# Optimization experiments

Hardware: AMD Instinct MI355X
Metric: run time of the kernel (lower is better)

The kernel has to match this reference:

```python
import jax, jax.numpy as jnp
import numpy as np

B, NZ, L = 8, 16, 512
E, DM, NH, HD = 256, 512, 16, 32
FF, NL, E1D, PDIM, PMAX = 1024, 8, 32, 64, 24
EPS_LN = 1e-5
EPS_D = 1e-12


def _ln(x, g, b):
    m = jnp.mean(x, axis=-1, keepdims=True)
    v = jnp.mean((x - m) ** 2, axis=-1, keepdims=True)
    return (x - m) / jnp.sqrt(v + EPS_LN) * g + b


def setup_inputs() -> dict:
    key = jax.random.key(0)
    ks = iter(jax.random.split(key, 32))
    rn = lambda shape, fan: jax.random.normal(next(ks), shape, jnp.float32) / np.float32(np.sqrt(fan))
    inp = {
        "z": jax.random.normal(next(ks), (B, NZ, L), jnp.float32),
        "x": jax.random.uniform(next(ks), (B, 20, L), jnp.float32),
        # embeddings
        "pos_table": rn((2 * PMAX + 1, PDIM), 1.0),
        "aa_table": rn((20, E1D), 1.0),
        # embed_x: Linear(nz,E), relu, Linear(E,E)
        "ex_w1": rn((NZ, E), NZ), "ex_b1": jnp.zeros((E,), jnp.float32),
        "ex_w2": rn((E, E), E), "ex_b2": jnp.zeros((E,), jnp.float32),
        # per-layer stacked params
        "Wq": rn((NL, E, DM), E), "Wk": rn((NL, E, DM), E), "Wv": rn((NL, E, DM), E),
        "Wo": rn((NL, DM, E), DM), "bo": jnp.zeros((NL, E), jnp.float32),
        "W2d": rn((NL, PDIM, NH), PDIM), "b2d": jnp.zeros((NL, NH), jnp.float32),
        "W1": rn((NL, E + E1D, FF), E + E1D), "b1": jnp.zeros((NL, FF), jnp.float32),
        "W2": rn((NL, FF, E), FF), "b2": jnp.zeros((NL, E), jnp.float32),
        "g1": jnp.ones((NL, E), jnp.float32), "be1": jnp.zeros((NL, E), jnp.float32),
        "g2": jnp.ones((NL, E), jnp.float32), "be2": jnp.zeros((NL, E), jnp.float32),
        # mlp_3d: Linear(E,E), relu, Linear(E,3)
        "m3_w1": rn((E, E), E), "m3_b1": jnp.zeros((E,), jnp.float32),
        "m3_w2": rn((E, 3), E), "m3_b2": jnp.zeros((3,), jnp.float32),
    }
    return inp


def reference(z, x, pos_table, aa_table, ex_w1, ex_b1, ex_w2, ex_b2,
              Wq, Wk, Wv, Wo, bo, W2d, b2d, W1, b1, W2, b2,
              g1, be1, g2, be2, m3_w1, m3_b1, m3_w2, m3_b2):
    Bn, _, Ln = z.shape
    h = jnp.transpose(z, (0, 2, 1))  # (B, L, nz)
    # relative-position bins: argmin over integer bins == clip to [-PMAX, PMAX]
    rel = jnp.arange(Ln)[None, :] - jnp.arange(Ln)[:, None]
    bins = jnp.clip(rel, -PMAX, PMAX) + PMAX
    pe = pos_table[bins]  # (L, L, PDIM), batch-replicated
    e_aa = aa_table[jnp.argmax(x, axis=1)]  # (B, L, E1D)
    # embed_x MLP
    h = jax.nn.relu(h @ ex_w1 + ex_b1) @ ex_w2 + ex_b2  # (B, L, E)
    scale = np.float32(1.0 / np.sqrt(DM))  # dp_attn_norm='d_model'
    for i in range(NL):
        q = (h @ Wq[i]).reshape(Bn, Ln, NH, HD) * scale
        k = (h @ Wk[i]).reshape(Bn, Ln, NH, HD)
        v = (h @ Wv[i]).reshape(Bn, Ln, NH, HD)
        # learned pairwise bias: mlp_2d then transpose(1,3).transpose(2,3) -> bias[h,i,j] = out[i,j,h]
        bias = jnp.einsum('lmp,ph->hlm', pe, W2d[i]) + b2d[i][:, None, None]
        scores = jnp.einsum('blhd,bmhd->bhlm', q, k) + bias[None]
        attn = jax.nn.softmax(scores, axis=-1)
        o = jnp.einsum('bhlm,bmhd->blhd', attn, v).reshape(Bn, Ln, DM)
        h = _ln(h + (o @ Wo[i] + bo[i]), g1[i], be1[i])
        um = jnp.concatenate([h, e_aa], axis=-1)  # (B, L, E+E1D)
        s2 = jax.nn.relu(um @ W1[i] + b1[i]) @ W2[i] + b2[i]
        h = _ln(h + s2, g2[i], be2[i])
    r = jax.nn.relu(h @ m3_w1 + m3_b1) @ m3_w2 + m3_b2  # (B, L, 3)
    # distance map (get_coords=False path)
    d = jnp.sqrt(jnp.sum((r[:, None, :, :] - r[:, :, None, :]) ** 2, axis=-1) + EPS_D)
    return d  # (B, L, L)
```

## Files before the change

### kernel.cpp

```cpp
#include <hip/hip_runtime.h>
#include <math.h>

constexpr int Bn = 8, NZ = 16, Ln = 512;
constexpr int E = 256, DM = 512, NH = 16, HD = 32;
constexpr int FF = 1024, NL = 8, E1D = 32, PDIM = 64, PMAX = 24;
constexpr int ROWS = Bn * Ln;
constexpr float QSCALE = 0.04419417382415922f;

typedef __attribute__((ext_vector_type(8))) short bf16x8;
typedef __attribute__((ext_vector_type(4))) float floatx4;

__device__ inline unsigned short f2b(float f) {
  union { float f; unsigned u; } v; v.f = f;
  unsigned r = (v.u + 0x7FFF + ((v.u >> 16) & 1)) >> 16;
  return (unsigned short)r;
}
__device__ inline float b2f(unsigned short u) {
  union { unsigned u; float f; } v; v.u = ((unsigned)u) << 16; return v.f;
}

__global__ __launch_bounds__(256) void transpose_qkv(
    const float* __restrict__ Wq, const float* __restrict__ Wk,
    const float* __restrict__ Wv, unsigned short* __restrict__ qkvT)
{
  __shared__ float t[32][33];
  int zb = blockIdx.z;
  int which = zb / NL, l = zb % NL;
  const float* s = (which == 0 ? Wq : which == 1 ? Wk : Wv) + (size_t)l * E * DM;
  unsigned short* d = qkvT + (size_t)l * 3 * DM * E + (size_t)which * DM * E;
  int c0 = blockIdx.x * 32, r0 = blockIdx.y * 32;
  int tx = threadIdx.x & 31, ty = threadIdx.x >> 5;
  #pragma unroll
  for (int i = 0; i < 4; ++i)
    t[ty + i * 8][tx] = s[(size_t)(r0 + ty + i * 8) * DM + c0 + tx];
  __syncthreads();
  #pragma unroll
  for (int i = 0; i < 4; ++i)
    d[(size_t)(c0 + ty + i * 8) * E + r0 + tx] = f2b(t[tx][ty + i * 8]);
}

__global__ __launch_bounds__(256) void transpose_bf16(
    const float* __restrict__ src, unsigned short* __restrict__ dst,
    int R, int C, size_t sls, size_t dls)
{
  __shared__ float t[32][33];
  int l = blockIdx.z;
  int c0 = blockIdx.x * 32, r0 = blockIdx.y * 32;
  int tx = threadIdx.x & 31, ty = threadIdx.x >> 5;
  const float* s = src + (size_t)l * sls;
  unsigned short* d = dst + (size_t)l * dls;
  #pragma unroll
  for (int i = 0; i < 4; ++i)
    t[ty + i * 8][tx] = s[(size_t)(r0 + ty + i * 8) * C + c0 + tx];
  __syncthreads();
  #pragma unroll
  for (int i = 0; i < 4; ++i)
    d[(size_t)(c0 + ty + i * 8) * R + r0 + tx] = f2b(t[tx][ty + i * 8]);
}

__global__ __launch_bounds__(256) void embed1_kernel(
    const float* __restrict__ z, const float* __restrict__ x,
    const float* __restrict__ aa,
    const float* __restrict__ w1, const float* __restrict__ b1,
    float* __restrict__ t0, unsigned short* __restrict__ umb)
{
  int row = blockIdx.x;
  int b = row >> 9, l = row & (Ln - 1);
  int t = threadIdx.x;
  __shared__ float zs[NZ];
  __shared__ int am_s;
  if (t < NZ) zs[t] = z[((size_t)b * NZ + t) * Ln + l];
  if (t == 0) {
    const float* xp = x + (size_t)b * 20 * Ln + l;
    int am = 0; float bv = xp[0];
    for (int c = 1; c < 20; ++c) { float vv = xp[(size_t)c * Ln]; if (vv > bv) { bv = vv; am = c; } }
    am_s = am;
  }
  __syncthreads();
  float a1 = b1[t];
  #pragma unroll
  for (int nz = 0; nz < NZ; ++nz) a1 += zs[nz] * w1[nz * E + t];
  t0[(size_t)row * E + t] = fmaxf(a1, 0.f);
  if (t < E1D) umb[(size_t)row * (E + E1D) + E + t] = f2b(aa[am_s * E1D + t]);
}

__global__ __launch_bounds__(256) void bias_kernel(
    const float* __restrict__ pos, const float* __restrict__ W2d,
    const float* __restrict__ b2d, float* __restrict__ bias49)
{
  int layer = blockIdx.x;
  for (int idx = threadIdx.x; idx < NH * 49; idx += 256) {
    int hh = idx / 49, bin = idx % 49;
    float acc = b2d[layer * NH + hh];
    for (int p = 0; p < PDIM; ++p)
      acc += pos[bin * PDIM + p] * W2d[((size_t)layer * PDIM + p) * NH + hh];
    bias49[(size_t)layer * NH * 49 + hh * 49 + bin] = acc;
  }
}

template<int BM, int BN, bool BIAS, bool RELU, bool OUTBF16, bool QKV>
__global__ __launch_bounds__(256) void gemm_mfma(
    const unsigned short* __restrict__ A, const unsigned short* __restrict__ Bt,
    const float* __restrict__ bias,
    float* __restrict__ Cf, unsigned short* __restrict__ Cb, int N, int K)
{
  constexpr int MT = BM / 32, NT = BN / 32;
  __shared__ __align__(16) unsigned short As[BM][40];
  __shared__ __align__(16) unsigned short Bs[BN][40];
  const int tid = threadIdx.x;
  const int wave = tid >> 6, ln = tid & 63;
  const int quad = ln >> 4, l16 = ln & 15;
  const int wm = wave >> 1, wn = wave & 1;
  const int m0 = blockIdx.y * BM, n0 = blockIdx.x * BN;

  floatx4 acc[MT][NT] = {};

  for (int kb = 0; kb < K; kb += 32) {
    __syncthreads();
    #pragma unroll
    for (int it = 0; it < BM / 64; ++it) {
      int c = tid + it * 256;
      int row = c >> 2, cc = (c & 3) * 8;
      *(float4*)&As[row][cc] = *(const float4*)(A + (size_t)(m0 + row) * K + kb + cc);
    }
    #pragma unroll
    for (int it = 0; it < BN / 64; ++it) {
      int c = tid + it * 256;
      int row = c >> 2, cc = (c & 3) * 8;
      *(float4*)&Bs[row][cc] = *(const float4*)(Bt + (size_t)(n0 + row) * K + kb + cc);
    }
    __syncthreads();
    bf16x8 af[MT], bfr[NT];
    #pragma unroll
    for (int i = 0; i < MT; ++i)
      af[i] = *(const bf16x8*)&As[wm * (BM / 2) + i * 16 + l16][quad * 8];
    #pragma unroll
    for (int j = 0; j < NT; ++j)
      bfr[j] = *(const bf16x8*)&Bs[wn * (BN / 2) + j * 16 + l16][quad * 8];
    #pragma unroll
    for (int i = 0; i < MT; ++i)
      #pragma unroll
      for (int j = 0; j < NT; ++j)
        acc[i][j] = __builtin_amdgcn_mfma_f32_16x16x32_bf16(af[i], bfr[j], acc[i][j], 0, 0, 0);
  }

  #pragma unroll
  for (int i = 0; i < MT; ++i)
    #pragma unroll
    for (int j = 0; j < NT; ++j) {
      int col = n0 + wn * (BN / 2) + j * 16 + l16;
      float bv = BIAS ? bias[col] : 0.f;
      float sc = QKV ? (col < 512 ? QSCALE : 1.f) : 1.f;
      #pragma unroll
      for (int r = 0; r < 4; ++r) {
        int rowg = m0 + wm * (BM / 2) + i * 16 + quad * 4 + r;
        float v = acc[i][j][r] * sc + bv;
        if (RELU) v = fmaxf(v, 0.f);
        if (OUTBF16) Cb[(size_t)rowg * N + col] = f2b(v);
        else Cf[(size_t)rowg * N + col] = v;
      }
    }
}

__global__ __launch_bounds__(256) void gemm_n256(
    const unsigned short* __restrict__ A, const unsigned short* __restrict__ Bt,
    const float* __restrict__ bias, const float* __restrict__ resid,
    float* __restrict__ Cf, int K)
{
  __shared__ __align__(16) unsigned short As[32][72];
  __shared__ __align__(16) unsigned short Bs[32][72];
  const int tid = threadIdx.x;
  const int wave = tid >> 6, ln = tid & 63;
  const int quad = ln >> 4, l16 = ln & 15;
  const int wm = wave >> 1, wn = wave & 1;
  const int m0 = blockIdx.y * 32, n0 = blockIdx.x * 32;
  const int srow = tid >> 3, scol = (tid & 7) * 8;

  floatx4 acc = {};

  for (int kb = 0; kb < K; kb += 64) {
    float4 ta = *(const float4*)(A + (size_t)(m0 + srow) * K + kb + scol);
    float4 tb = *(const float4*)(Bt + (size_t)(n0 + srow) * K + kb + scol);
    __syncthreads();
    *(float4*)&As[srow][scol] = ta;
    *(float4*)&Bs[srow][scol] = tb;
    __syncthreads();
    #pragma unroll
    for (int kc = 0; kc < 2; ++kc) {
      bf16x8 af = *(const bf16x8*)&As[wm * 16 + l16][kc * 32 + quad * 8];
      bf16x8 bf = *(const bf16x8*)&Bs[wn * 16 + l16][kc * 32 + quad * 8];
      acc = __builtin_amdgcn_mfma_f32_16x16x32_bf16(af, bf, acc, 0, 0, 0);
    }
  }

  const int col = n0 + wn * 16 + l16;
  const float bv = bias[col];
  #pragma unroll
  for (int r = 0; r < 4; ++r) {
    int rowg = m0 + wm * 16 + quad * 4 + r;
    Cf[(size_t)rowg * 256 + col] = acc[r] + bv + resid[(size_t)rowg * 256 + col];
  }
}

__global__ __launch_bounds__(256) void attn_kernel(
    const unsigned short* __restrict__ qkv, const float* __restrict__ bias49,
    unsigned short* __restrict__ o)
{
  const int i0 = blockIdx.x * 64;
  const int bh = blockIdx.y;
  const int b = bh >> 4, hh = bh & 15;
  const int tid = threadIdx.x;
  const int wave = tid >> 6, ln = tid & 63;
  const int quad = ln >> 4, l16 = ln & 15;

  __shared__ __align__(16) unsigned short Kt[64][40];
  __shared__ __align__(16) unsigned short Vt[32][72];
  __shared__ __align__(16) unsigned short Pw[4][2][16][72];
  __shared__ float bsh[49];

  if (tid < 49) bsh[tid] = bias49[hh * 49 + tid];

  const unsigned short* qkvb = qkv + (size_t)b * Ln * 1536;

  const int qrow = i0 + wave * 16 + l16;
  const bf16x8 qf = *(const bf16x8*)(qkvb + (size_t)qrow * 1536 + hh * 32 + quad * 8);

  float m[4], l[4];
  #pragma unroll
  for (int r = 0; r < 4; ++r) { m[r] = -1e30f; l[r] = 0.f; }
  floatx4 acc_o[2] = {};

  const int krow = tid >> 2, kch = (tid & 3) * 8;
  const int vkey = tid & 63, vch = (tid >> 6) * 8;

  for (int jt = 0; jt < 8; ++jt) {
    const int j0 = jt * 64;
    __syncthreads();
    *(float4*)&Kt[krow][kch] =
        *(const float4*)(qkvb + (size_t)(j0 + krow) * 1536 + 512 + hh * 32 + kch);
    bf16x8 vv = *(const bf16x8*)(qkvb + (size_t)(j0 + vkey) * 1536 + 1024 + hh * 32 + vch);
    #pragma unroll
    for (int i = 0; i < 8; ++i) Vt[vch + i][vkey] = (unsigned short)vv[i];
    __syncthreads();

    floatx4 s4[4];
    #pragma unroll
    for (int t = 0; t < 4; ++t) {
      bf16x8 kf = *(const bf16x8*)&Kt[16 * t + l16][quad * 8];
      s4[t] = __builtin_amdgcn_mfma_f32_16x16x32_bf16(qf, kf, (floatx4){0.f, 0.f, 0.f, 0.f}, 0, 0, 0);
    }
    const int relmin = j0 - (i0 + 63), relmax = j0 + 63 - i0;
    if (relmin >= PMAX) {
      float bc = bsh[48];
      #pragma unroll
      for (int t = 0; t < 4; ++t)
        #pragma unroll
        for (int r = 0; r < 4; ++r) s4[t][r] += bc;
    } else if (relmax <= -PMAX) {
      float bc = bsh[0];
      #pragma unroll
      for (int t = 0; t < 4; ++t)
        #pragma unroll
        for (int r = 0; r < 4; ++r) s4[t][r] += bc;
    } else {
      const int base_rel = (j0 + l16) - (i0 + wave * 16 + quad * 4);
      #pragma unroll
      for (int t = 0; t < 4; ++t)
        #pragma unroll
        for (int r = 0; r < 4; ++r) {
          int rel = base_rel + 16 * t - r;
          rel = rel < -PMAX ? -PMAX : (rel > PMAX ? PMAX : rel);
          s4[t][r] += bsh[rel + PMAX];
        }
    }

    float mloc[4], alpha[4], psum[4];
    #pragma unroll
    for (int r = 0; r < 4; ++r) {
      mloc[r] = fmaxf(fmaxf(s4[0][r], s4[1][r]), fmaxf(s4[2][r], s4[3][r]));
      #pragma unroll
      for (int off = 1; off < 16; off <<= 1)
        mloc[r] = fmaxf(mloc[r], __shfl_xor(mloc[r], off, 64));
      float mnew = fmaxf(m[r], mloc[r]);
      alpha[r] = __expf(m[r] - mnew);
      m[r] = mnew;
      psum[r] = 0.f;
    }
    #pragma unroll
    for (int t = 0; t < 4; ++t)
      #pragma unroll
      for (int r = 0; r < 4; ++r) {
        float p = __expf(s4[t][r] - m[r]);
        s4[t][r] = p;
        psum[r] += p;
      }
    #pragma unroll
    for (int r = 0; r < 4; ++r) {
      #pragma unroll
      for (int off = 1; off < 16; off <<= 1)
        psum[r] += __shfl_xor(psum[r], off, 64);
      l[r] = l[r] * alpha[r] + psum[r];
      acc_o[0][r] *= alpha[r];
      acc_o[1][r] *= alpha[r];
    }

    #pragma unroll
    for (int t = 0; t < 4; ++t)
      #pragma unroll
      for (int r = 0; r < 4; ++r) {
        float p = s4[t][r];
        unsigned short hi = f2b(p);
        unsigned short lo = f2b(p - b2f(hi));
        Pw[wave][0][quad * 4 + r][16 * t + l16] = hi;
        Pw[wave][1][quad * 4 + r][16 * t + l16] = lo;
      }

    #pragma unroll
    for (int kh = 0; kh < 2; ++kh) {
      bf16x8 phi = *(const bf16x8*)&Pw[wave][0][l16][kh * 32 + quad * 8];
      bf16x8 plo = *(const bf16x8*)&Pw[wave][1][l16][kh * 32 + quad * 8];
      #pragma unroll
      for (int nt = 0; nt < 2; ++nt) {
        bf16x8 vf = *(const bf16x8*)&Vt[nt * 16 + l16][kh * 32 + quad * 8];
        acc_o[nt] = __builtin_amdgcn_mfma_f32_16x16x32_bf16(phi, vf, acc_o[nt], 0, 0, 0);
        acc_o[nt] = __builtin_amdgcn_mfma_f32_16x16x32_bf16(plo, vf, acc_o[nt], 0, 0, 0);
      }
    }
  }

  #pragma unroll
  for (int r = 0; r < 4; ++r) {
    float inv = 1.f / l[r];
    size_t rowg = (size_t)b * Ln + i0 + wave * 16 + quad * 4 + r;
    #pragma unroll
    for (int nt = 0; nt < 2; ++nt)
      o[rowg * 512 + hh * 32 + nt * 16 + l16] = f2b(acc_o[nt][r] * inv);
  }
}

__global__ __launch_bounds__(256) void ln_kernel(
    const float* __restrict__ xin, const float* __restrict__ g,
    const float* __restrict__ be, float* __restrict__ hout,
    unsigned short* __restrict__ bout, int bstride)
{
  int row = blockIdx.x, t = threadIdx.x;
  float v = xin[(size_t)row * E + t];
  float s = v;
  #pragma unroll
  for (int off = 32; off > 0; off >>= 1) s += __shfl_down(s, off, 64);
  __shared__ float ws4[4];
  __shared__ float mbc, rbc;
  if ((t & 63) == 0) ws4[t >> 6] = s;
  __syncthreads();
  if (t == 0) mbc = (ws4[0] + ws4[1] + ws4[2] + ws4[3]) * (1.f / E);
  __syncthreads();
  float m = mbc;
  float d = v - m;
  float s2 = d * d;
  #pragma unroll
  for (int off = 32; off > 0; off >>= 1) s2 += __shfl_down(s2, off, 64);
  if ((t & 63) == 0) ws4[t >> 6] = s2;
  __syncthreads();
  if (t == 0) rbc = rsqrtf((ws4[0] + ws4[1] + ws4[2] + ws4[3]) * (1.f / E) + 1e-5f);
  __syncthreads();
  float y = d * rbc * g[t] + be[t];
  hout[(size_t)row * E + t] = y;
  bout[(size_t)row * bstride + t] = f2b(y);
}

template<bool RELU, bool BIAS, bool MIRROR>
__global__ __launch_bounds__(256) void gemm64f(
    const float* __restrict__ A, const float* __restrict__ B,
    const float* __restrict__ bias, float* __restrict__ C,
    unsigned short* __restrict__ mir, int N, int K)
{
  __shared__ __align__(16) float As[16][64];
  __shared__ __align__(16) float Bss[16][68];
  const int tid = threadIdx.x;
  const int tx = tid & 15, ty = tid >> 4;
  const int m0 = blockIdx.y * 64, n0 = blockIdx.x * 64;
  const int arow = tid >> 2, acol = (tid & 3) * 4;
  const int brow = tid >> 6, bcol = tid & 63;
  float acc[4][4] = {};
  for (int kb = 0; kb < K; kb += 16) {
    __syncthreads();
    float4 av = *(const float4*)(A + (size_t)(m0 + arow) * K + kb + acol);
    As[acol + 0][arow] = av.x; As[acol + 1][arow] = av.y;
    As[acol + 2][arow] = av.z; As[acol + 3][arow] = av.w;
    #pragma unroll
    for (int kk = 0; kk < 4; ++kk)
      Bss[brow + kk * 4][bcol] = B[(size_t)(kb + brow + kk * 4) * N + n0 + bcol];
    __syncthreads();
    #pragma unroll
    for (int k = 0; k < 16; ++k) {
      float4 a = *(const float4*)&As[k][4 * ty];
      float4 b = *(const float4*)&Bss[k][4 * tx];
      float av4[4] = {a.x, a.y, a.z, a.w};
      float bv4[4] = {b.x, b.y, b.z, b.w};
      #pragma unroll
      for (int ii = 0; ii < 4; ++ii)
        #pragma unroll
        for (int jj = 0; jj < 4; ++jj)
          acc[ii][jj] += av4[ii] * bv4[jj];
    }
  }
  #pragma unroll
  for (int ii = 0; ii < 4; ++ii) {
    size_t row = (size_t)m0 + 4 * ty + ii;
    int col = n0 + 4 * tx;
    float4 vv;
    vv.x = acc[ii][0]; vv.y = acc[ii][1]; vv.z = acc[ii][2]; vv.w = acc[ii][3];
    if (BIAS) {
      float4 bb = *(const float4*)(bias + col);
      vv.x += bb.x; vv.y += bb.y; vv.z += bb.z; vv.w += bb.w;
    }
    if (RELU) {
      vv.x = fmaxf(vv.x, 0.f); vv.y = fmaxf(vv.y, 0.f);
      vv.z = fmaxf(vv.z, 0.f); vv.w = fmaxf(vv.w, 0.f);
    }
    *(float4*)(C + row * N + col) = vv;
    if (MIRROR) {
      ushort4 mv;
      mv.x = f2b(vv.x); mv.y = f2b(vv.y); mv.z = f2b(vv.z); mv.w = f2b(vv.w);
      *(ushort4*)(mir + row * N + col) = mv;
    }
  }
}

__global__ __launch_bounds__(256) void final_r_kernel(
    const float* __restrict__ t1, const float* __restrict__ w2,
    const float* __restrict__ b2, float* __restrict__ r)
{
  int row = blockIdx.x, t = threadIdx.x;
  float xv = t1[(size_t)row * E + t];
  float p0 = xv * w2[t * 3 + 0];
  float p1 = xv * w2[t * 3 + 1];
  float p2 = xv * w2[t * 3 + 2];
  #pragma unroll
  for (int off = 32; off > 0; off >>= 1) {
    p0 += __shfl_down(p0, off, 64);
    p1 += __shfl_down(p1, off, 64);
    p2 += __shfl_down(p2, off, 64);
  }
  __shared__ float red[4][3];
  if ((t & 63) == 0) { int w = t >> 6; red[w][0] = p0; red[w][1] = p1; red[w][2] = p2; }
  __syncthreads();
  if (t < 3)
    r[(size_t)row * 3 + t] = red[0][t] + red[1][t] + red[2][t] + red[3][t] + b2[t];
}

__global__ __launch_bounds__(512) void dist_kernel(
    const float* __restrict__ r, float* __restrict__ out)
{
  int bi = blockIdx.x;
  int j = threadIdx.x;
  int b = bi >> 9;
  float x0 = r[(size_t)bi * 3 + 0];
  float y0 = r[(size_t)bi * 3 + 1];
  float z0 = r[(size_t)bi * 3 + 2];
  const float* rj = r + ((size_t)b * Ln + j) * 3;
  float dx = rj[0] - x0, dy = rj[1] - y0, dz = rj[2] - z0;
  out[(size_t)bi * Ln + j] = sqrtf(dx * dx + dy * dy + dz * dz + 1e-12f);
}

extern "C" void kernel_launch(void* const* d_in, const int* in_sizes, int n_in,
                              void* d_out, int out_size, void* d_ws, size_t ws_size,
                              hipStream_t stream)
{
  const float* z     = (const float*)d_in[0];
  const float* x     = (const float*)d_in[1];
  const float* pos   = (const float*)d_in[2];
  const float* aa    = (const float*)d_in[3];
  const float* ex_w1 = (const float*)d_in[4];
  const float* ex_b1 = (const float*)d_in[5];
  const float* ex_w2 = (const float*)d_in[6];
  const float* ex_b2 = (const float*)d_in[7];
  const float* Wq    = (const float*)d_in[8];
  const float* Wk    = (const float*)d_in[9];
  const float* Wv    = (const float*)d_in[10];
  const float* Wo    = (const float*)d_in[11];
  const float* bo    = (const float*)d_in[12];
  const float* W2d   = (const float*)d_in[13];
  const float* b2d   = (const float*)d_in[14];
  const float* W1    = (const float*)d_in[15];
  const float* b1    = (const float*)d_in[16];
  const float* W2    = (const float*)d_in[17];
  const float* b2    = (const float*)d_in[18];
  const float* g1    = (const float*)d_in[19];
  const float* be1   = (const float*)d_in[20];
  const float* g2    = (const float*)d_in[21];
  const float* be2   = (const float*)d_in[22];
  const float* m3w1  = (const float*)d_in[23];
  const float* m3b1  = (const float*)d_in[24];
  const float* m3w2  = (const float*)d_in[25];
  const float* m3b2  = (const float*)d_in[26];

  float* ws     = (float*)d_ws;
  float* h      = ws;
  float* t0     = h + (size_t)ROWS * E;
  float* r      = t0 + (size_t)ROWS * E;
  float* bias49 = r + (size_t)ROWS * 3;
  unsigned short* us = (unsigned short*)(bias49 + NL * NH * 49);
  unsigned short* hb   = us;
  unsigned short* umb  = hb  + (size_t)ROWS * E;
  unsigned short* qkvb = umb + (size_t)ROWS * (E + E1D);
  unsigned short* ob   = qkvb + (size_t)ROWS * 3 * DM;
  unsigned short* t1b  = ob  + (size_t)ROWS * DM;
  unsigned short* qkvT = t1b + (size_t)ROWS * FF;
  unsigned short* WoT  = qkvT + (size_t)NL * 3 * DM * E;
  unsigned short* W1T  = WoT  + (size_t)NL * E * DM;
  unsigned short* W2T  = W1T  + (size_t)NL * FF * (E+E1D);
  float* tmp = t0;
  float* t1f = (float*)t1b;

  transpose_qkv<<<dim3(DM/32, E/32, 3*NL), 256, 0, stream>>>(Wq, Wk, Wv, qkvT);
  transpose_bf16<<<dim3(E/32, DM/32, NL), 256, 0, stream>>>(
      Wo, WoT, DM, E, (size_t)DM * E, (size_t)DM * E);
  transpose_bf16<<<dim3(FF/32, (E+E1D)/32, NL), 256, 0, stream>>>(
      W1, W1T, E + E1D, FF, (size_t)(E+E1D) * FF, (size_t)(E+E1D) * FF);
  transpose_bf16<<<dim3(E/32, FF/32, NL), 256, 0, stream>>>(
      W2, W2T, FF, E, (size_t)FF * E, (size_t)FF * E);

  embed1_kernel<<<ROWS, 256, 0, stream>>>(z, x, aa, ex_w1, ex_b1, t0, umb);
  gemm64f<false,true,true><<<dim3(E/64, ROWS/64), 256, 0, stream>>>(
      t0, ex_w2, ex_b2, h, hb, E, E);
  bias_kernel<<<NL, 256, 0, stream>>>(pos, W2d, b2d, bias49);

  for (int i = 0; i < NL; ++i) {
    gemm_mfma<128,128,false,false,true,true><<<dim3(12, 32), 256, 0, stream>>>(
        hb, qkvT + (size_t)i * 3 * DM * E, nullptr, nullptr, qkvb, 3 * DM, E);
    attn_kernel<<<dim3(Ln/64, Bn*NH), 256, 0, stream>>>(
        qkvb, bias49 + (size_t)i * NH * 49, ob);
    gemm_n256<<<dim3(E/32, ROWS/32), 256, 0, stream>>>(
        ob, WoT + (size_t)i * DM * E, bo + (size_t)i * E, h, tmp, DM);
    ln_kernel<<<ROWS, 256, 0, stream>>>(tmp, g1 + (size_t)i * E, be1 + (size_t)i * E, h, umb, E + E1D);
    gemm_mfma<128,128,true,true,true,false><<<dim3(FF/128, ROWS/128), 256, 0, stream>>>(
        umb, W1T + (size_t)i * FF * (E+E1D), b1 + (size_t)i * FF, nullptr, t1b, FF, E + E1D);
    gemm_n256<<<dim3(E/32, ROWS/32), 256, 0, stream>>>(
        t1b, W2T + (size_t)i * E * FF, b2 + (size_t)i * E, h, tmp, FF);
    ln_kernel<<<ROWS, 256, 0, stream>>>(tmp, g2 + (size_t)i * E, be2 + (size_t)i * E, h, hb, E);
  }

  gemm64f<true,true,false><<<dim3(E/64, ROWS/64), 256, 0, stream>>>(
      h, m3w1, m3b1, t1f, nullptr, E, E);
  final_r_kernel<<<ROWS, 256, 0, stream>>>(t1f, m3w2, m3b2, r);
  dist_kernel<<<ROWS, 512, 0, stream>>>(r, (float*)d_out);
}
```

Before: 906.1 us.

## Prefetch next K-tile into registers and remap GEMM blocks across XCDs

Both MFMA GEMM kernels now load the next K-slice from global memory into registers while the current slice is in shared memory, so load latency overlaps the MFMA work. The QKV and FFN1 GEMMs switch from 128x128 to 64x128 tiles, doubling the block count for better CU occupancy. gemm_n256 uses a 1D grid with an XCD-aware mapping so that blocks on the same XCD share rows of A in L2. The cost is extra register pressure from the prefetch buffers, and the hardcoded mapping assumes 1024 blocks over 8 XCDs.

```diff
diff --git a/kernel.cpp b/kernel.cpp
--- a/kernel.cpp
+++ b/kernel.cpp
@@ -105,6 +105,7 @@
     float* __restrict__ Cf, unsigned short* __restrict__ Cb, int N, int K)
 {
   constexpr int MT = BM / 32, NT = BN / 32;
+  constexpr int AIT = BM / 64, BIT = BN / 64;
   __shared__ __align__(16) unsigned short As[BM][40];
   __shared__ __align__(16) unsigned short Bs[BN][40];
   const int tid = threadIdx.x;
@@ -115,19 +116,41 @@
 
   floatx4 acc[MT][NT] = {};
 
+  float4 pa[AIT], pb[BIT];
+  #pragma unroll
+  for (int it = 0; it < AIT; ++it) {
+    int c = tid + it * 256; int row = c >> 2, cc = (c & 3) * 8;
+    pa[it] = *(const float4*)(A + (size_t)(m0 + row) * K + cc);
+  }
+  #pragma unroll
+  for (int it = 0; it < BIT; ++it) {
+    int c = tid + it * 256; int row = c >> 2, cc = (c & 3) * 8;
+    pb[it] = *(const float4*)(Bt + (size_t)(n0 + row) * K + cc);
+  }
+
   for (int kb = 0; kb < K; kb += 32) {
     __syncthreads();
     #pragma unroll
-    for (int it = 0; it < BM / 64; ++it) {
-      int c = tid + it * 256;
-      int row = c >> 2, cc = (c & 3) * 8;
-      *(float4*)&As[row][cc] = *(const float4*)(A + (size_t)(m0 + row) * K + kb + cc);
-    }
-    #pragma unroll
-    for (int it = 0; it < BN / 64; ++it) {
-      int c = tid + it * 256;
-      int row = c >> 2, cc = (c & 3) * 8;
-      *(float4*)&Bs[row][cc] = *(const float4*)(Bt + (size_t)(n0 + row) * K + kb + cc);
+    for (int it = 0; it < AIT; ++it) {
+      int c = tid + it * 256; int row = c >> 2, cc = (c & 3) * 8;
+      *(float4*)&As[row][cc] = pa[it];
+    }
+    #pragma unroll
+    for (int it = 0; it < BIT; ++it) {
+      int c = tid + it * 256; int row = c >> 2, cc = (c & 3) * 8;
+      *(float4*)&Bs[row][cc] = pb[it];
+    }
+    if (kb + 32 < K) {
+      #pragma unroll
+      for (int it = 0; it < AIT; ++it) {
+        int c = tid + it * 256; int row = c >> 2, cc = (c & 3) * 8;
+        pa[it] = *(const float4*)(A + (size_t)(m0 + row) * K + kb + 32 + cc);
+      }
+      #pragma unroll
+      for (int it = 0; it < BIT; ++it) {
+        int c = tid + it * 256; int row = c >> 2, cc = (c & 3) * 8;
+        pb[it] = *(const float4*)(Bt + (size_t)(n0 + row) * K + kb + 32 + cc);
+      }
     }
     __syncthreads();
     bf16x8 af[MT], bfr[NT];
@@ -173,17 +196,24 @@
   const int wave = tid >> 6, ln = tid & 63;
   const int quad = ln >> 4, l16 = ln & 15;
   const int wm = wave >> 1, wn = wave & 1;
-  const int m0 = blockIdx.y * 32, n0 = blockIdx.x * 32;
+  const int id = blockIdx.x;
+  const int xcd = id & 7, idx = id >> 3;
+  const int m0 = (xcd * 16 + (idx & 15)) * 32;
+  const int n0 = (idx >> 4) * 32;
   const int srow = tid >> 3, scol = (tid & 7) * 8;
 
   floatx4 acc = {};
+  float4 ta = *(const float4*)(A + (size_t)(m0 + srow) * K + scol);
+  float4 tb = *(const float4*)(Bt + (size_t)(n0 + srow) * K + scol);
 
   for (int kb = 0; kb < K; kb += 64) {
-    float4 ta = *(const float4*)(A + (size_t)(m0 + srow) * K + kb + scol);
-    float4 tb = *(const float4*)(Bt + (size_t)(n0 + srow) * K + kb + scol);
     __syncthreads();
     *(float4*)&As[srow][scol] = ta;
     *(float4*)&Bs[srow][scol] = tb;
+    if (kb + 64 < K) {
+      ta = *(const float4*)(A + (size_t)(m0 + srow) * K + kb + 64 + scol);
+      tb = *(const float4*)(Bt + (size_t)(n0 + srow) * K + kb + 64 + scol);
+    }
     __syncthreads();
     #pragma unroll
     for (int kc = 0; kc < 2; ++kc) {
@@ -527,16 +557,16 @@
   bias_kernel<<<NL, 256, 0, stream>>>(pos, W2d, b2d, bias49);
 
   for (int i = 0; i < NL; ++i) {
-    gemm_mfma<128,128,false,false,true,true><<<dim3(12, 32), 256, 0, stream>>>(
+    gemm_mfma<64,128,false,false,true,true><<<dim3(12, 64), 256, 0, stream>>>(
         hb, qkvT + (size_t)i * 3 * DM * E, nullptr, nullptr, qkvb, 3 * DM, E);
     attn_kernel<<<dim3(Ln/64, Bn*NH), 256, 0, stream>>>(
         qkvb, bias49 + (size_t)i * NH * 49, ob);
-    gemm_n256<<<dim3(E/32, ROWS/32), 256, 0, stream>>>(
+    gemm_n256<<<1024, 256, 0, stream>>>(
         ob, WoT + (size_t)i * DM * E, bo + (size_t)i * E, h, tmp, DM);
     ln_kernel<<<ROWS, 256, 0, stream>>>(tmp, g1 + (size_t)i * E, be1 + (size_t)i * E, h, umb, E + E1D);
-    gemm_mfma<128,128,true,true,true,false><<<dim3(FF/128, ROWS/128), 256, 0, stream>>>(
+    gemm_mfma<64,128,true,true,true,false><<<dim3(FF/128, 64), 256, 0, stream>>>(
         umb, W1T + (size_t)i * FF * (E+E1D), b1 + (size_t)i * FF, nullptr, t1b, FF, E + E1D);
-    gemm_n256<<<dim3(E/32, ROWS/32), 256, 0, stream>>>(
+    gemm_n256<<<1024, 256, 0, stream>>>(
         t1b, W2T + (size_t)i * E * FF, b2 + (size_t)i * E, h, tmp, FF);
     ln_kernel<<<ROWS, 256, 0, stream>>>(tmp, g2 + (size_t)i * E, be2 + (size_t)i * E, h, hb, E);
   }
```

Result: slower. 990.1 us (+9.3%).
